# Kernel optimization log

Hardware: AMD Instinct MI355X
Metric: run time of the kernel (lower is better)

## Reference

```python
import jax, jax.numpy as jnp
import numpy as np

QS = 64  # quantization block size (quantization_shape)


def setup_inputs() -> dict:
    key = jax.random.key(0)
    x = jax.random.normal(key, (4, 4096, 4096), dtype=jnp.float32)
    return {"x": x}


def reference(x) -> jnp.ndarray:
    # Forward of EfficientMemorySiLU is exactly F.silu(x); the per-block
    # quantization only affects what is saved for backward, not the output.
    return x * jax.nn.sigmoid(x)
```

## Files before the change

kernel.cpp:

```cpp
#include <hip/hip_runtime.h>
#include <hip/hip_bf16.h>


__global__ __launch_bounds__(256) void silu_f32x4_kernel(const float4* __restrict__ x,
                                                         float4* __restrict__ out,
                                                         int n4) {
    int i = blockIdx.x * blockDim.x + threadIdx.x;
    if (i >= n4) return;
    float4 v = x[i];
    float4 r;
    r.x = v.x / (1.0f + __expf(-v.x));
    r.y = v.y / (1.0f + __expf(-v.y));
    r.z = v.z / (1.0f + __expf(-v.z));
    r.w = v.w / (1.0f + __expf(-v.w));
    out[i] = r;
}

extern "C" void kernel_launch(void* const* d_in, const int* in_sizes, int n_in,
                              void* d_out, int out_size, void* d_ws, size_t ws_size,
                              hipStream_t stream) {
    const float* x = (const float*)d_in[0];
    float* out = (float*)d_out;
    int n = in_sizes[0];
    int n4 = n / 4;

    const int block = 256;
    int grid = (n4 + block - 1) / block;

    silu_f32x4_kernel<<<grid, block, 0, stream>>>(
        (const float4*)x, (float4*)out, n4);
}
```

Baseline: 411.1 us.

## Process four float4 per thread with nontemporal loads/stores and fast reciprocal

Measured after the change: 415.3 us. Within noise of the previous version (+1.0%).

```diff
diff --git a/kernel.cpp b/kernel.cpp
--- a/kernel.cpp
+++ b/kernel.cpp
@@ -2,18 +2,33 @@
 #include <hip/hip_bf16.h>
 
 
-__global__ __launch_bounds__(256) void silu_f32x4_kernel(const float4* __restrict__ x,
-                                                         float4* __restrict__ out,
-                                                         int n4) {
-    int i = blockIdx.x * blockDim.x + threadIdx.x;
-    if (i >= n4) return;
-    float4 v = x[i];
-    float4 r;
-    r.x = v.x / (1.0f + __expf(-v.x));
-    r.y = v.y / (1.0f + __expf(-v.y));
-    r.z = v.z / (1.0f + __expf(-v.z));
-    r.w = v.w / (1.0f + __expf(-v.w));
-    out[i] = r;
+typedef float f32x4 __attribute__((ext_vector_type(4)));
+
+__global__ __launch_bounds__(256) void silu_f32x4x4_kernel(const f32x4* __restrict__ x,
+                                                           f32x4* __restrict__ out,
+                                                           int n4) {
+    int base = blockIdx.x * (256 * 4) + threadIdx.x;
+
+    f32x4 v[4];
+#pragma unroll
+    for (int k = 0; k < 4; ++k) {
+        int idx = base + k * 256;
+        if (idx < n4) v[k] = __builtin_nontemporal_load(&x[idx]);
+    }
+
+#pragma unroll
+    for (int k = 0; k < 4; ++k) {
+        int idx = base + k * 256;
+        if (idx < n4) {
+            f32x4 s = v[k];
+            f32x4 r;
+            r.x = s.x * __builtin_amdgcn_rcpf(1.0f + __expf(-s.x));
+            r.y = s.y * __builtin_amdgcn_rcpf(1.0f + __expf(-s.y));
+            r.z = s.z * __builtin_amdgcn_rcpf(1.0f + __expf(-s.z));
+            r.w = s.w * __builtin_amdgcn_rcpf(1.0f + __expf(-s.w));
+            __builtin_nontemporal_store(r, &out[idx]);
+        }
+    }
 }
 
 extern "C" void kernel_launch(void* const* d_in, const int* in_sizes, int n_in,
@@ -25,8 +40,9 @@
     int n4 = n / 4;
 
     const int block = 256;
-    int grid = (n4 + block - 1) / block;
+    const int per_block = block * 4;
+    int grid = (n4 + per_block - 1) / per_block;
 
-    silu_f32x4_kernel<<<grid, block, 0, stream>>>(
-        (const float4*)x, (float4*)out, n4);
+    silu_f32x4x4_kernel<<<grid, block, 0, stream>>>(
+        (const f32x4*)x, (f32x4*)out, n4);
 }
```
